# Optimization experiments

Hardware: AMD Instinct MI355X
Metric: run time of the kernel (lower is better)

The kernel has to match this reference:

```python
import jax, jax.numpy as jnp
import numpy as np

B, N, M = 16, 512, 512
VS, QS, OS, H = 2048, 1024, 2048, 16
DH = OS // H  # per-head dim


def setup_inputs() -> dict:
    key = jax.random.key(0)
    ks = jax.random.split(key, 8)
    s = lambda fan_in: 1.0 / np.sqrt(fan_in)
    return {
        "v": jax.random.normal(ks[0], (B, N, VS), jnp.float32),
        "q": jax.random.normal(ks[1], (B, M, QS), jnp.float32),
        "v_mask": jnp.ones((B, N), jnp.float32),
        "q_mask": jnp.ones((B, M), jnp.float32),
        "Wv": jax.random.normal(ks[2], (VS, 3 * OS), jnp.float32) * s(VS),
        "bv": jnp.zeros((3 * OS,), jnp.float32),
        "Wq": jax.random.normal(ks[3], (QS, 3 * OS), jnp.float32) * s(QS),
        "bq": jnp.zeros((3 * OS,), jnp.float32),
        "Wvo": jax.random.normal(ks[4], (OS + VS, OS), jnp.float32) * s(OS + VS),
        "bvo": jnp.zeros((OS,), jnp.float32),
        "Wqo": jax.random.normal(ks[5], (OS + QS, OS), jnp.float32) * s(OS + QS),
        "bqo": jnp.zeros((OS,), jnp.float32),
    }


def _heads(x):
    # [B, L, OS] -> [B, L, H, DH]; torch.split over dim 2 == contiguous head slices
    return x.reshape(x.shape[0], x.shape[1], H, DH)


def reference(v, q, v_mask, q_mask, Wv, bv, Wq, bq, Wvo, bvo, Wqo, bqo):
    # FCNet = relu(Linear)
    v_trans = jax.nn.relu(v @ Wv + bv) * v_mask[:, :, None]
    q_trans = jax.nn.relu(q @ Wq + bq) * q_mask[:, :, None]
    v_key, v_qry, v_val = (_heads(t) for t in jnp.split(v_trans, 3, axis=2))
    q_key, q_qry, q_val = (_heads(t) for t in jnp.split(q_trans, 3, axis=2))
    scale = 1.0 / np.sqrt(DH)
    neg_inf = jnp.float32(-jnp.inf)

    # q2v: visual queries attend over question keys -> [B, H, N, M]
    q2v = jnp.einsum("bnhd,bmhd->bhnm", v_qry, q_key) * scale
    q2v = jnp.where(q_mask[:, None, None, :] == 0, neg_inf, q2v)
    v_update = jnp.einsum("bhnm,bmhd->bnhd", jax.nn.softmax(q2v, axis=-1), q_val)
    v_update = v_update.reshape(B, N, OS)

    # v2q: question queries attend over visual keys -> [B, H, M, N]
    v2q = jnp.einsum("bmhd,bnhd->bhmn", q_qry, v_key) * scale
    v2q = jnp.where(v_mask[:, None, None, :] == 0, neg_inf, v2q)
    q_update = jnp.einsum("bhmn,bnhd->bmhd", jax.nn.softmax(v2q, axis=-1), v_val)
    q_update = q_update.reshape(B, M, OS)

    updated_v = jax.nn.relu(jnp.concatenate([v, v_update], axis=2) @ Wvo + bvo)
    updated_q = jax.nn.relu(jnp.concatenate([q, q_update], axis=2) @ Wqo + bqo)
    return updated_v, updated_q
```

## Files before the change

### kernel.cpp

```cpp
#include <hip/hip_runtime.h>
#include <hip/hip_bf16.h>
#include <cstdint>


typedef __hip_bfloat16 bf16;
typedef __attribute__((ext_vector_type(8))) __bf16 bf16x8;
typedef __attribute__((ext_vector_type(4))) float f32x4;
typedef __attribute__((ext_vector_type(4))) unsigned short us4;
typedef __attribute__((ext_vector_type(8))) unsigned short us8;

#define AS1 __attribute__((address_space(1)))
#define AS3 __attribute__((address_space(3)))

__device__ __forceinline__ void gl_lds16(const bf16* g, bf16* l) {
    __builtin_amdgcn_global_load_lds((AS1 void*)(uintptr_t)(g), (AS3 void*)(l), 16, 0, 0);
}

__device__ __forceinline__ bf16x8 ld8(const bf16* p) { return *(const bf16x8*)p; }

__device__ __forceinline__ f32x4 mfma16(bf16x8 a, bf16x8 b, f32x4 c) {
    return __builtin_amdgcn_mfma_f32_16x16x32_bf16(a, b, c, 0, 0, 0);
}

__device__ __forceinline__ unsigned short f2bs(float f) {
    unsigned u = __builtin_bit_cast(unsigned, f);
    unsigned r = u + 0x7FFFu + ((u >> 16) & 1u);
    return (unsigned short)(r >> 16);
}

__global__ __launch_bounds__(256) void cvt_cols_k(
    const float* __restrict__ src, bf16* __restrict__ dst,
    int cprShift, int dstStride, int totalChunks)
{
    const int id = blockIdx.x * 256 + threadIdx.x;
    if (id >= totalChunks) return;
    const int row = id >> cprShift;
    const int cc = (id - (row << cprShift)) << 3;
    const float* s = src + ((size_t)row << (cprShift + 3)) + cc;
    const float4 a = *(const float4*)s;
    const float4 b = *(const float4*)(s + 4);
    us8 o;
    o[0] = f2bs(a.x); o[1] = f2bs(a.y); o[2] = f2bs(a.z); o[3] = f2bs(a.w);
    o[4] = f2bs(b.x); o[5] = f2bs(b.y); o[6] = f2bs(b.z); o[7] = f2bs(b.w);
    *(us8*)(dst + (size_t)row * dstStride + cc) = o;
}

__global__ __launch_bounds__(256) void cvt_transpose_k(
    const float* __restrict__ in, unsigned short* __restrict__ out,
    int inStride, int outStride)
{
    __shared__ unsigned short tile[64][65];
    const int ti = blockIdx.x * 64;
    const int tj = blockIdx.y * 64;
    const int t = threadIdx.x;
    const int r = t >> 4;
    const int c4 = (t & 15) << 2;
#pragma unroll
    for (int i = 0; i < 4; ++i) {
        const float4 v = *(const float4*)(in + (size_t)(tj + r + i * 16) * inStride + ti + c4);
        tile[r + i * 16][c4 + 0] = f2bs(v.x);
        tile[r + i * 16][c4 + 1] = f2bs(v.y);
        tile[r + i * 16][c4 + 2] = f2bs(v.z);
        tile[r + i * 16][c4 + 3] = f2bs(v.w);
    }
    __syncthreads();
#pragma unroll
    for (int i = 0; i < 4; ++i) {
        const int orow = ti + r + i * 16;
        us4 v;
        v[0] = tile[c4 + 0][r + i * 16];
        v[1] = tile[c4 + 1][r + i * 16];
        v[2] = tile[c4 + 2][r + i * 16];
        v[3] = tile[c4 + 3][r + i * 16];
        *(us4*)(out + (size_t)orow * outStride + tj + c4) = v;
    }
}

__global__ __launch_bounds__(256) void transpose_k(
    const unsigned short* __restrict__ in, unsigned short* __restrict__ out,
    int inStride, int outStride, size_t inOffB, int inOffH, size_t outSliceStride)
{
    __shared__ unsigned short tile[64][65];
    const int z = blockIdx.z;
    const unsigned short* inp = in + (size_t)(z >> 4) * inOffB + (size_t)(z & 15) * inOffH;
    unsigned short* outp = out + (size_t)z * outSliceStride;
    const int ti = blockIdx.x * 64;
    const int tj = blockIdx.y * 64;
    const int t = threadIdx.x;
    const int r = t >> 4;
    const int c4 = (t & 15) << 2;
#pragma unroll
    for (int i = 0; i < 4; ++i) {
        us4 v = *(const us4*)(inp + (size_t)(tj + r + i * 16) * inStride + ti + c4);
        tile[r + i * 16][c4 + 0] = v[0];
        tile[r + i * 16][c4 + 1] = v[1];
        tile[r + i * 16][c4 + 2] = v[2];
        tile[r + i * 16][c4 + 3] = v[3];
    }
    __syncthreads();
#pragma unroll
    for (int i = 0; i < 4; ++i) {
        const int orow = ti + r + i * 16;
        us4 v;
        v[0] = tile[c4 + 0][r + i * 16];
        v[1] = tile[c4 + 1][r + i * 16];
        v[2] = tile[c4 + 2][r + i * 16];
        v[3] = tile[c4 + 3][r + i * 16];
        *(us4*)(outp + (size_t)orow * outStride + tj + c4) = v;
    }
}

template <typename OutT>
__global__ __launch_bounds__(512, 2) void gemm_bt(
    const bf16* __restrict__ A, const bf16* __restrict__ BT,
    const float* __restrict__ bias, const float* __restrict__ mask,
    OutT* __restrict__ C, int K, int lda, int ldb, int ldc)
{
    __shared__ __align__(16) bf16 smem[49152];
    const int tid = threadIdx.x;
    const int lane = tid & 63;
    const int l16 = lane & 15;
    const int quad = lane >> 4;
    const int wave = tid >> 6;
    const int wm = wave >> 2;
    const int wn = wave & 3;
    const int rofs = ((quad ^ ((l16 >> 1) & 3)) << 3);
    const size_t row0 = (size_t)blockIdx.y * 256;
    const size_t col0 = (size_t)blockIdx.x * 256;

    const int ci0 = tid, ci1 = 512 + tid;
    const int ra0 = ci0 >> 2, ja0 = ci0 & 3;
    const int ra1 = ci1 >> 2, ja1 = ci1 & 3;
    const bf16* Asrc0 = A + (row0 + ra0) * lda + ((ja0 ^ ((ra0 >> 1) & 3)) << 3);
    const bf16* Asrc1 = A + (row0 + ra1) * lda + ((ja1 ^ ((ra1 >> 1) & 3)) << 3);
    const bf16* Bsrc0 = BT + (col0 + ra0) * ldb + ((ja0 ^ ((ra0 >> 1) & 3)) << 3);
    const bf16* Bsrc1 = BT + (col0 + ra1) * ldb + ((ja1 ^ ((ra1 >> 1) & 3)) << 3);

    bf16* b0 = smem;
    bf16* b1 = smem + 16384;
    bf16* b2 = smem + 32768;

    const f32x4 z4 = {0.f, 0.f, 0.f, 0.f};
    f32x4 acc[8][4];
#pragma unroll
    for (int r = 0; r < 8; ++r)
#pragma unroll
        for (int c = 0; c < 4; ++c) acc[r][c] = z4;

    const int nt = K >> 5;

    gl_lds16(Asrc0, b0 + ci0 * 8);
    gl_lds16(Asrc1, b0 + ci1 * 8);
    gl_lds16(Bsrc0, b0 + 8192 + ci0 * 8);
    gl_lds16(Bsrc1, b0 + 8192 + ci1 * 8);
    gl_lds16(Asrc0 + 32, b1 + ci0 * 8);
    gl_lds16(Asrc1 + 32, b1 + ci1 * 8);
    gl_lds16(Bsrc0 + 32, b1 + 8192 + ci0 * 8);
    gl_lds16(Bsrc1 + 32, b1 + 8192 + ci1 * 8);
    asm volatile("s_waitcnt vmcnt(4)" ::: "memory");
    __builtin_amdgcn_s_barrier();
    asm volatile("" ::: "memory");

    bf16* cur = b0; bf16* nxt = b1; bf16* nx2 = b2;
    for (int t = 0; t < nt; ++t) {
        const bool st = (t + 2) < nt;
        const int kofs = (t + 2) << 5;
        const bf16* aRd = cur + (wm * 128 + l16) * 32 + rofs;
        const bf16* bRd = cur + 8192 + (wn * 64 + l16) * 32 + rofs;

        bf16x8 bfr[4], af[4], af2[4];
#pragma unroll
        for (int fc = 0; fc < 4; ++fc) bfr[fc] = ld8(bRd + fc * 512);
#pragma unroll
        for (int fr = 0; fr < 4; ++fr) af[fr] = ld8(aRd + fr * 512);
#pragma unroll
        for (int fr = 0; fr < 4; ++fr) af2[fr] = ld8(aRd + 2048 + fr * 512);

        if (st) {
            gl_lds16(Asrc0 + kofs, nx2 + ci0 * 8);
            gl_lds16(Asrc1 + kofs, nx2 + ci1 * 8);
            gl_lds16(Bsrc0 + kofs, nx2 + 8192 + ci0 * 8);
            gl_lds16(Bsrc1 + kofs, nx2 + 8192 + ci1 * 8);
        }

        __builtin_amdgcn_s_setprio(1);
#pragma unroll
        for (int fr = 0; fr < 4; ++fr)
#pragma unroll
            for (int fc = 0; fc < 4; ++fc)
                acc[fr][fc] = mfma16(af[fr], bfr[fc], acc[fr][fc]);
#pragma unroll
        for (int fr = 0; fr < 4; ++fr)
#pragma unroll
            for (int fc = 0; fc < 4; ++fc)
                acc[fr + 4][fc] = mfma16(af2[fr], bfr[fc], acc[fr + 4][fc]);
        __builtin_amdgcn_s_setprio(0);

        if (t + 1 < nt) {
            if (st) asm volatile("s_waitcnt vmcnt(4)" ::: "memory");
            else    asm volatile("s_waitcnt vmcnt(0)" ::: "memory");
            __builtin_amdgcn_s_barrier();
            asm volatile("" ::: "memory");
        }
        bf16* tmp = cur; cur = nxt; nxt = nx2; nx2 = tmp;
    }

    asm volatile("" ::: "memory");
    __syncthreads();

    float bcol[4];
#pragma unroll
    for (int fc = 0; fc < 4; ++fc) bcol[fc] = bias[col0 + wn * 64 + fc * 16 + l16];

    if constexpr (sizeof(OutT) == 2) {
        unsigned short* stg = (unsigned short*)smem;
#pragma unroll
        for (int p = 0; p < 8; ++p) {
            if (wm == (p >> 2)) {
#pragma unroll
                for (int d = 0; d < 2; ++d) {
                    const int fr = (p & 3) * 2 + d;
#pragma unroll
                    for (int fc = 0; fc < 4; ++fc) {
                        const int lcol = wn * 64 + fc * 16 + l16;
#pragma unroll
                        for (int g = 0; g < 4; ++g) {
                            const int lrow = d * 16 + quad * 4 + g;
                            const size_t grow = row0 + (size_t)p * 32 + lrow;
                            float v = acc[fr][fc][g] + bcol[fc];
                            v = v > 0.f ? v : 0.f;
                            if (mask) v *= mask[grow];
                            stg[lrow * 264 + lcol] = f2bs(v);
                        }
                    }
                }
            }
            asm volatile("" ::: "memory");
            __syncthreads();
            const int srow = tid >> 4;
            const int scol = (tid & 15) * 16;
            const us8 o0 = *(const us8*)(stg + srow * 264 + scol);
            const us8 o1 = *(const us8*)(stg + srow * 264 + scol + 8);
            OutT* dst = C + (row0 + p * 32 + srow) * ldc + col0 + scol;
            *(us8*)dst = o0;
            *(us8*)(dst + 8) = o1;
            __syncthreads();
        }
    } else {
        float* stg = (float*)smem;
#pragma unroll
        for (int p = 0; p < 8; ++p) {
            if (wm == (p >> 2)) {
#pragma unroll
                for (int d = 0; d < 2; ++d) {
                    const int fr = (p & 3) * 2 + d;
#pragma unroll
                    for (int fc = 0; fc < 4; ++fc) {
                        const int lcol = wn * 64 + fc * 16 + l16;
#pragma unroll
                        for (int g = 0; g < 4; ++g) {
                            const int lrow = d * 16 + quad * 4 + g;
                            const size_t grow = row0 + (size_t)p * 32 + lrow;
                            float v = acc[fr][fc][g] + bcol[fc];
                            v = v > 0.f ? v : 0.f;
                            if (mask) v *= mask[grow];
                            stg[lrow * 260 + lcol] = v;
                        }
                    }
                }
            }
            asm volatile("" ::: "memory");
            __syncthreads();
            const int srow = tid >> 4;
            const int scol = (tid & 15) * 16;
            float* dst = (float*)C + (row0 + p * 32 + srow) * ldc + col0 + scol;
            const float* s = stg + srow * 260 + scol;
            *(f32x4*)(dst + 0)  = *(const f32x4*)(s + 0);
            *(f32x4*)(dst + 4)  = *(const f32x4*)(s + 4);
            *(f32x4*)(dst + 8)  = *(const f32x4*)(s + 8);
            *(f32x4*)(dst + 12) = *(const f32x4*)(s + 12);
            __syncthreads();
        }
    }
}

__global__ __launch_bounds__(128) void attn_k(
    const bf16* __restrict__ Q, const bf16* __restrict__ Kk,
    const bf16* __restrict__ VT, const float* __restrict__ kmask,
    bf16* __restrict__ Out,
    int Lq, int Lk, int qStride, int kStride, int outStride, int outColOff)
{
    const int bh = blockIdx.y;
    const int b = bh >> 4, h = bh & 15;
    const int n0 = blockIdx.x * 32;
    const int tid = threadIdx.x;
    const int wave = tid >> 6, lane = tid & 63;
    const int l16 = lane & 15, quad = lane >> 4;

    __shared__ __align__(16) bf16 smem[16640 + 8192];
    bf16* kv = smem + 16640;

#pragma unroll
    for (int i = 0; i < 4; ++i) {
        const int e = i * 1024 + tid * 8;
        const int r = e >> 7, d = e & 127;
        gl_lds16(Q + (size_t)(b * Lq + n0 + r) * qStride + h * 128 + d, smem + e);
    }
    __syncthreads();

    bf16x8 aq[4];
#pragma unroll
    for (int ks = 0; ks < 4; ++ks)
        aq[ks] = ld8(smem + (wave * 16 + l16) * 128 + ks * 32 + quad * 8);
    __syncthreads();

    const bf16* Kb = Kk + (size_t)b * Lk * kStride + h * 128;
    f32x4 S[32];
    const int swz = (l16 & 7);
#pragma unroll
    for (int kt = 0; kt < 8; ++kt) {
#pragma unroll
        for (int c = 0; c < 8; ++c) {
            const int e = c * 1024 + tid * 8;
            const int r = e >> 7;
            const int j = (e >> 3) & 15;
            gl_lds16(Kb + (size_t)(kt * 64 + r) * kStride + ((j ^ (r & 7)) << 3), kv + e);
        }
        __syncthreads();
        __builtin_amdgcn_s_setprio(1);
#pragma unroll
        for (int tt = 0; tt < 4; ++tt) {
            const int row = tt * 16 + l16;
            f32x4 c2 = {0.f, 0.f, 0.f, 0.f};
#pragma unroll
            for (int ks = 0; ks < 4; ++ks)
                c2 = mfma16(aq[ks], ld8(kv + row * 128 + (((ks * 4 + quad) ^ swz) << 3)), c2);
            S[kt * 4 + tt] = c2;
        }
        __builtin_amdgcn_s_setprio(0);
        __syncthreads();
    }

    const float scale = 0.08838834764831845f;
    float mx[4] = {-3.0e38f, -3.0e38f, -3.0e38f, -3.0e38f};
#pragma unroll
    for (int t = 0; t < 32; ++t)
#pragma unroll
        for (int g = 0; g < 4; ++g) mx[g] = fmaxf(mx[g], S[t][g]);
#pragma unroll
    for (int off = 1; off < 16; off <<= 1)
#pragma unroll
        for (int g = 0; g < 4; ++g) mx[g] = fmaxf(mx[g], __shfl_xor(mx[g], off));

    float sm[4] = {0.f, 0.f, 0.f, 0.f};
    const float* mrow = kmask + (size_t)b * Lk;
#pragma unroll
    for (int t = 0; t < 32; ++t) {
        const float mv = mrow[t * 16 + l16];
#pragma unroll
        for (int g = 0; g < 4; ++g) {
            float p = (mv != 0.f) ? __expf((S[t][g] - mx[g]) * scale) : 0.f;
            S[t][g] = p;
            sm[g] += p;
        }
    }
#pragma unroll
    for (int off = 1; off < 16; off <<= 1)
#pragma unroll
        for (int g = 0; g < 4; ++g) sm[g] += __shfl_xor(sm[g], off);
    float rs[4];
#pragma unroll
    for (int g = 0; g < 4; ++g) rs[g] = 1.f / sm[g];

    bf16* pw = smem + wave * 8320;
#pragma unroll
    for (int t = 0; t < 32; ++t) {
        const int col = t * 16 + l16;
#pragma unroll
        for (int g = 0; g < 4; ++g)
            pw[(quad * 4 + g) * 520 + col] = __float2bfloat16(S[t][g] * rs[g]);
    }
    asm volatile("" ::: "memory");
    __syncthreads();

    bf16x8 pa[16];
#pragma unroll
    for (int ks = 0; ks < 16; ++ks)
        pa[ks] = ld8(pw + l16 * 520 + ks * 32 + quad * 8);

    const bf16* Vb = VT + (size_t)bh * 128 * Lk;
    const size_t orow = (size_t)b * Lq + n0 + wave * 16 + quad * 4;
    for (int dt = 0; dt < 8; ++dt) {
#pragma unroll
        for (int c = 0; c < 8; ++c) {
            const int e = c * 1024 + tid * 8;
            const int r = e >> 9;
            const int j = (e >> 3) & 63;
            gl_lds16(Vb + (size_t)(dt * 16 + r) * Lk + ((j ^ (r & 7)) << 3), kv + e);
        }
        __syncthreads();
        __builtin_amdgcn_s_setprio(1);
        f32x4 c2 = {0.f, 0.f, 0.f, 0.f};
#pragma unroll
        for (int ks = 0; ks < 16; ++ks)
            c2 = mfma16(pa[ks], ld8(kv + l16 * 512 + (((ks * 4 + quad) ^ swz) << 3)), c2);
        __builtin_amdgcn_s_setprio(0);
        const int col = outColOff + h * 128 + dt * 16 + l16;
#pragma unroll
        for (int g = 0; g < 4; ++g)
            Out[(orow + g) * outStride + col] = __float2bfloat16(c2[g]);
        __syncthreads();
    }
}

extern "C" void kernel_launch(void* const* d_in, const int* in_sizes, int n_in,
                              void* d_out, int out_size, void* d_ws, size_t ws_size,
                              hipStream_t stream)
{
    (void)in_sizes; (void)n_in; (void)out_size; (void)ws_size;
    const float* v   = (const float*)d_in[0];
    const float* q   = (const float*)d_in[1];
    const float* vm  = (const float*)d_in[2];
    const float* qm  = (const float*)d_in[3];
    const float* Wv  = (const float*)d_in[4];
    const float* bv  = (const float*)d_in[5];
    const float* Wq  = (const float*)d_in[6];
    const float* bq  = (const float*)d_in[7];
    const float* Wvo = (const float*)d_in[8];
    const float* bvo = (const float*)d_in[9];
    const float* Wqo = (const float*)d_in[10];
    const float* bqo = (const float*)d_in[11];

    float* out_v = (float*)d_out;
    float* out_q = out_v + (size_t)8192 * 2048;

    bf16* ws = (bf16*)d_ws;
    bf16* v_trans = ws; ws += (size_t)8192 * 6144;
    bf16* q_trans = ws; ws += (size_t)8192 * 6144;
    bf16* vcat    = ws; ws += (size_t)8192 * 4096;
    bf16* qcat    = ws; ws += (size_t)8192 * 3072;
    bf16* WvT     = ws; ws += (size_t)6144 * 2048;
    bf16* WqT     = ws; ws += (size_t)6144 * 1024;
    bf16* WvoT    = ws; ws += (size_t)2048 * 4096;
    bf16* WqoT    = ws; ws += (size_t)2048 * 3072;
    bf16* VvalT   = ws; ws += (size_t)256 * 128 * 512;
    bf16* QvalT   = ws; ws += (size_t)256 * 128 * 512;

    cvt_cols_k<<<8192, 256, 0, stream>>>(v, vcat, 8, 4096, 8192 * 256);
    cvt_cols_k<<<4096, 256, 0, stream>>>(q, qcat, 7, 3072, 8192 * 128);

    cvt_transpose_k<<<dim3(96, 32), 256, 0, stream>>>(Wv,  (unsigned short*)WvT,  6144, 2048);
    cvt_transpose_k<<<dim3(96, 16), 256, 0, stream>>>(Wq,  (unsigned short*)WqT,  6144, 1024);
    cvt_transpose_k<<<dim3(32, 64), 256, 0, stream>>>(Wvo, (unsigned short*)WvoT, 2048, 4096);
    cvt_transpose_k<<<dim3(32, 48), 256, 0, stream>>>(Wqo, (unsigned short*)WqoT, 2048, 3072);

    gemm_bt<bf16><<<dim3(24, 32), 512, 0, stream>>>(vcat, WvT, bv, vm, v_trans, 2048, 4096, 2048, 6144);
    gemm_bt<bf16><<<dim3(24, 32), 512, 0, stream>>>(qcat, WqT, bq, qm, q_trans, 1024, 3072, 1024, 6144);

    transpose_k<<<dim3(2, 8, 256), 256, 0, stream>>>((const unsigned short*)(v_trans + 4096), (unsigned short*)VvalT,
                                                     6144, 512, (size_t)512 * 6144, 128, 65536);
    transpose_k<<<dim3(2, 8, 256), 256, 0, stream>>>((const unsigned short*)(q_trans + 4096), (unsigned short*)QvalT,
                                                     6144, 512, (size_t)512 * 6144, 128, 65536);

    attn_k<<<dim3(16, 256), 128, 0, stream>>>(v_trans + 2048, q_trans, QvalT, qm, vcat,
                                              512, 512, 6144, 6144, 4096, 2048);
    attn_k<<<dim3(16, 256), 128, 0, stream>>>(q_trans + 2048, v_trans, VvalT, vm, qcat,
                                              512, 512, 6144, 6144, 3072, 1024);

    gemm_bt<float><<<dim3(8, 32), 512, 0, stream>>>(vcat, WvoT, bvo, nullptr, out_v, 4096, 4096, 4096, 2048);
    gemm_bt<float><<<dim3(8, 32), 512, 0, stream>>>(qcat, WqoT, bqo, nullptr, out_q, 3072, 3072, 3072, 2048);
}
```

Baseline: 1.352 ms.

## Restructure GEMM mainloop into 8-slot ping-pong schedule with fine-grained barriers

Replaces the triple-buffered K=32 mainloop with an 8-slot LDS layout covering two 64-wide K tiles. Each K half is split into separate A and B slots, and LDS reads, global-to-LDS prefetches and MFMA bursts are interleaved with many barriers, in the style of an HipKittens-like 8-wave ping-pong. The goal is better overlap of memory traffic with MFMA work. In exchange LDS use grows to 128KB, which may reduce occupancy below two blocks per CU. It also assumes K is a multiple of 128 and adds many barriers.

```diff
diff --git a/kernel.cpp b/kernel.cpp
--- a/kernel.cpp
+++ b/kernel.cpp
@@ -116,7 +116,7 @@
     const float* __restrict__ bias, const float* __restrict__ mask,
     OutT* __restrict__ C, int K, int lda, int ldb, int ldc)
 {
-    __shared__ __align__(16) bf16 smem[49152];
+    __shared__ __align__(16) bf16 smem[65536];
     const int tid = threadIdx.x;
     const int lane = tid & 63;
     const int l16 = lane & 15;
@@ -128,17 +128,12 @@
     const size_t row0 = (size_t)blockIdx.y * 256;
     const size_t col0 = (size_t)blockIdx.x * 256;
 
-    const int ci0 = tid, ci1 = 512 + tid;
-    const int ra0 = ci0 >> 2, ja0 = ci0 & 3;
-    const int ra1 = ci1 >> 2, ja1 = ci1 & 3;
-    const bf16* Asrc0 = A + (row0 + ra0) * lda + ((ja0 ^ ((ra0 >> 1) & 3)) << 3);
-    const bf16* Asrc1 = A + (row0 + ra1) * lda + ((ja1 ^ ((ra1 >> 1) & 3)) << 3);
-    const bf16* Bsrc0 = BT + (col0 + ra0) * ldb + ((ja0 ^ ((ra0 >> 1) & 3)) << 3);
-    const bf16* Bsrc1 = BT + (col0 + ra1) * ldb + ((ja1 ^ ((ra1 >> 1) & 3)) << 3);
-
-    bf16* b0 = smem;
-    bf16* b1 = smem + 16384;
-    bf16* b2 = smem + 32768;
+    const int r0 = tid >> 2;
+    const int jg0 = (((tid & 3) ^ ((r0 >> 1) & 3)) << 3);
+    const bf16* pA = A + (row0 + r0) * lda + jg0;
+    const bf16* pB = BT + (col0 + r0) * ldb + jg0;
+    const size_t lda128 = (size_t)128 * lda;
+    const size_t ldb128 = (size_t)128 * ldb;
 
     const f32x4 z4 = {0.f, 0.f, 0.f, 0.f};
     f32x4 acc[8][4];
@@ -147,63 +142,95 @@
 #pragma unroll
         for (int c = 0; c < 4; ++c) acc[r][c] = z4;
 
-    const int nt = K >> 5;
-
-    gl_lds16(Asrc0, b0 + ci0 * 8);
-    gl_lds16(Asrc1, b0 + ci1 * 8);
-    gl_lds16(Bsrc0, b0 + 8192 + ci0 * 8);
-    gl_lds16(Bsrc1, b0 + 8192 + ci1 * 8);
-    gl_lds16(Asrc0 + 32, b1 + ci0 * 8);
-    gl_lds16(Asrc1 + 32, b1 + ci1 * 8);
-    gl_lds16(Bsrc0 + 32, b1 + 8192 + ci0 * 8);
-    gl_lds16(Bsrc1 + 32, b1 + 8192 + ci1 * 8);
-    asm volatile("s_waitcnt vmcnt(4)" ::: "memory");
-    __builtin_amdgcn_s_barrier();
-    asm volatile("" ::: "memory");
-
-    bf16* cur = b0; bf16* nxt = b1; bf16* nx2 = b2;
-    for (int t = 0; t < nt; ++t) {
-        const bool st = (t + 2) < nt;
-        const int kofs = (t + 2) << 5;
-        const bf16* aRd = cur + (wm * 128 + l16) * 32 + rofs;
-        const bf16* bRd = cur + 8192 + (wn * 64 + l16) * 32 + rofs;
-
-        bf16x8 bfr[4], af[4], af2[4];
-#pragma unroll
-        for (int fc = 0; fc < 4; ++fc) bfr[fc] = ld8(bRd + fc * 512);
-#pragma unroll
-        for (int fr = 0; fr < 4; ++fr) af[fr] = ld8(aRd + fr * 512);
-#pragma unroll
-        for (int fr = 0; fr < 4; ++fr) af2[fr] = ld8(aRd + 2048 + fr * 512);
-
-        if (st) {
-            gl_lds16(Asrc0 + kofs, nx2 + ci0 * 8);
-            gl_lds16(Asrc1 + kofs, nx2 + ci1 * 8);
-            gl_lds16(Bsrc0 + kofs, nx2 + 8192 + ci0 * 8);
-            gl_lds16(Bsrc1 + kofs, nx2 + 8192 + ci1 * 8);
-        }
-
-        __builtin_amdgcn_s_setprio(1);
-#pragma unroll
-        for (int fr = 0; fr < 4; ++fr)
-#pragma unroll
-            for (int fc = 0; fc < 4; ++fc)
-                acc[fr][fc] = mfma16(af[fr], bfr[fc], acc[fr][fc]);
-#pragma unroll
-        for (int fr = 0; fr < 4; ++fr)
-#pragma unroll
-            for (int fc = 0; fc < 4; ++fc)
-                acc[fr + 4][fc] = mfma16(af2[fr], bfr[fc], acc[fr + 4][fc]);
-        __builtin_amdgcn_s_setprio(0);
-
-        if (t + 1 < nt) {
-            if (st) asm volatile("s_waitcnt vmcnt(4)" ::: "memory");
-            else    asm volatile("s_waitcnt vmcnt(0)" ::: "memory");
-            __builtin_amdgcn_s_barrier();
-            asm volatile("" ::: "memory");
-        }
-        bf16* tmp = cur; cur = nxt; nxt = nx2; nx2 = tmp;
-    }
+    const int NT = K >> 6;
+    const int NI = NT >> 1;
+
+#define STG_A(SL, TT, KH) do { \
+    gl_lds16(pA + (TT) * 64 + (KH) * 32, smem + (SL) * 8192 + tid * 8); \
+    gl_lds16(pA + lda128 + (TT) * 64 + (KH) * 32, smem + (SL) * 8192 + 4096 + tid * 8); \
+} while (0)
+#define STG_B(SL, TT, KH) do { \
+    gl_lds16(pB + (TT) * 64 + (KH) * 32, smem + (SL) * 8192 + tid * 8); \
+    gl_lds16(pB + ldb128 + (TT) * 64 + (KH) * 32, smem + (SL) * 8192 + 4096 + tid * 8); \
+} while (0)
+#define LDA4(SL, RH) \
+    _Pragma("unroll") \
+    for (int j = 0; j < 4; ++j) \
+        af[j] = ld8(smem + (SL) * 8192 + (wm * 128 + (RH) * 64 + j * 16 + l16) * 32 + rofs);
+#define LDB4(SL) \
+    _Pragma("unroll") \
+    for (int j = 0; j < 4; ++j) \
+        bfr[j] = ld8(smem + (SL) * 8192 + (wn * 64 + j * 16 + l16) * 32 + rofs);
+#define MM16(RH) \
+    __builtin_amdgcn_s_setprio(1); \
+    _Pragma("unroll") \
+    for (int j = 0; j < 4; ++j) \
+        _Pragma("unroll") \
+        for (int c = 0; c < 4; ++c) \
+            acc[(RH) * 4 + j][c] = mfma16(af[j], bfr[c], acc[(RH) * 4 + j][c]); \
+    __builtin_amdgcn_s_setprio(0);
+#define BARR() do { asm volatile("" ::: "memory"); __builtin_amdgcn_s_barrier(); asm volatile("" ::: "memory"); } while (0)
+
+    STG_B(2, 0, 0); STG_A(0, 0, 0); STG_B(3, 0, 1); STG_A(1, 0, 1);
+    STG_B(6, 1, 0); STG_A(4, 1, 0); STG_B(7, 1, 1);
+    asm volatile("s_waitcnt vmcnt(6)" ::: "memory");
+    BARR();
+
+    bf16x8 af[4], bfr[4];
+
+    for (int i = 0; i < NI; ++i) {
+        const int U = 2 * i;
+        const bool st = (U + 2) < NT;
+        LDB4(2); LDA4(0, 0);
+        STG_A(5, U + 1, 1);
+        BARR();
+        MM16(0);
+        BARR();
+        LDA4(0, 1);
+        if (st) STG_B(2, U + 2, 0);
+        BARR();
+        MM16(1);
+        BARR();
+        LDB4(3); LDA4(1, 0);
+        if (st) STG_A(0, U + 2, 0);
+        BARR();
+        MM16(0);
+        BARR();
+        LDA4(1, 1);
+        if (st) STG_B(3, U + 2, 1);
+        BARR();
+        MM16(1);
+        if (st) asm volatile("s_waitcnt vmcnt(6)" ::: "memory");
+        else    asm volatile("s_waitcnt vmcnt(0)" ::: "memory");
+        BARR();
+        LDB4(6); LDA4(4, 0);
+        if (st) STG_A(1, U + 2, 1);
+        BARR();
+        MM16(0);
+        BARR();
+        LDA4(4, 1);
+        if (st) STG_B(6, U + 3, 0);
+        BARR();
+        MM16(1);
+        BARR();
+        LDB4(7); LDA4(5, 0);
+        if (st) STG_A(4, U + 3, 0);
+        BARR();
+        MM16(0);
+        BARR();
+        LDA4(5, 1);
+        if (st) STG_B(7, U + 3, 1);
+        BARR();
+        MM16(1);
+        if (st) asm volatile("s_waitcnt vmcnt(6)" ::: "memory");
+        BARR();
+    }
+#undef STG_A
+#undef STG_B
+#undef LDA4
+#undef LDB4
+#undef MM16
+#undef BARR
 
     asm volatile("" ::: "memory");
     __syncthreads();
```

Measured after the change: 1.372 ms. No clear change (+1.5%).
